# Kernel tuning notes

Measured on AMD Instinct MI355X. Metric: run time of the kernel, lower is better.

Reference implementation:

```python
import jax, jax.numpy as jnp
import numpy as np

B, L, S, H, E, D = 4, 2048, 2048, 8, 64, 64

def setup_inputs() -> dict:
    key = jax.random.key(0)
    kq, kk, kv = jax.random.split(key, 3)
    queries = jax.random.normal(kq, (B, L, H, E), dtype=jnp.float32)
    keys = jax.random.normal(kk, (B, S, H, E), dtype=jnp.float32)
    values = jax.random.normal(kv, (B, S, H, D), dtype=jnp.float32)
    return {"queries": queries, "keys": keys, "values": values}

def reference(queries, keys, values):
    # scale = self.scale or 1/sqrt(E)
    scale = 1.0 / jnp.sqrt(jnp.float32(queries.shape[-1]))
    # scores: [B, H, L, S]
    scores = jnp.einsum('blhe,bshe->bhls', queries, keys)
    # dropout is identity at inference (Keras Dropout only active in training)
    A = jax.nn.softmax(scale * scores, axis=-1)
    # output: [B, L, H, D]
    return jnp.einsum('bhls,bshd->blhd', A, values)
```

## Files before the change

kernel.cpp:

```cpp
#include <hip/hip_runtime.h>


#define B_ 4
#define L_ 2048
#define S_ 2048
#define H_ 8

#define NUMSZ (B_ * L_ * H_ * 64)
#define LSZ (B_ * L_ * H_)
#define KVELEM (B_ * H_ * S_ * 64)
#define TILE_ELEMS 2048

typedef __attribute__((ext_vector_type(8))) __bf16 bf16x8;
typedef __attribute__((ext_vector_type(4))) __bf16 bf16x4;
typedef __attribute__((ext_vector_type(16))) float floatx16;

union BF4U { bf16x4 v; uint2 u; };
union BF8U { bf16x8 v; uint4 u; };

__device__ __forceinline__ void async_load16(const void* g, void* l) {
  __builtin_amdgcn_global_load_lds(
      (const __attribute__((address_space(1))) unsigned int*)g,
      (__attribute__((address_space(3))) unsigned int*)l, 16, 0, 0);
}

__device__ __forceinline__ bf16x8 cvt8(float4 a, float4 b) {
  bf16x8 r;
  r[0] = (__bf16)a.x; r[1] = (__bf16)a.y; r[2] = (__bf16)a.z; r[3] = (__bf16)a.w;
  r[4] = (__bf16)b.x; r[5] = (__bf16)b.y; r[6] = (__bf16)b.z; r[7] = (__bf16)b.w;
  return r;
}

__device__ __forceinline__ void softmax_pb(const floatx16& sc, int h32, float& l,
                                           bf16x8& pB0v, bf16x8& pB1v) {
  BF4U pg[4];
#pragma unroll
  for (int g = 0; g < 4; ++g) {
    float p0 = __builtin_amdgcn_exp2f(sc[4 * g + 0]);
    float p1 = __builtin_amdgcn_exp2f(sc[4 * g + 1]);
    float p2 = __builtin_amdgcn_exp2f(sc[4 * g + 2]);
    float p3 = __builtin_amdgcn_exp2f(sc[4 * g + 3]);
    l += (p0 + p1) + (p2 + p3);
    pg[g].v = (bf16x4){(__bf16)p0, (__bf16)p1, (__bf16)p2, (__bf16)p3};
  }
  uint2 sendA = h32 ? pg[0].u : pg[1].u;
  uint2 sendB = h32 ? pg[2].u : pg[3].u;
  uint2 recvA, recvB;
  recvA.x = __shfl_xor((int)sendA.x, 32);
  recvA.y = __shfl_xor((int)sendA.y, 32);
  recvB.x = __shfl_xor((int)sendB.x, 32);
  recvB.y = __shfl_xor((int)sendB.y, 32);
  BF8U pB0, pB1;
  if (h32 == 0) {
    pB0.u = (uint4){pg[0].u.x, pg[0].u.y, recvA.x, recvA.y};
    pB1.u = (uint4){pg[2].u.x, pg[2].u.y, recvB.x, recvB.y};
  } else {
    pB0.u = (uint4){recvA.x, recvA.y, pg[1].u.x, pg[1].u.y};
    pB1.u = (uint4){recvB.x, recvB.y, pg[3].u.x, pg[3].u.y};
  }
  pB0v = pB0.v;
  pB1v = pB1.v;
}

__global__ __launch_bounds__(256) void prep_kernel(const float* __restrict__ K,
                                                   const float* __restrict__ V,
                                                   __bf16* __restrict__ Kb,
                                                   __bf16* __restrict__ Vb) {
  __shared__ float Vs[32 * 64];
  const int bid = blockIdx.x;
  const int xcd = bid & 7;
  const int idx = bid >> 3;
  const int pair = xcd * 4 + (idx >> 6);
  const int tile = idx & 63;
  const int h = pair & 7;
  const int b = pair >> 3;
  const int obid = pair * 64 + tile;
  const int s0 = tile * 32;
  const int i = threadIdx.x;

  {
    const int s = i >> 3, cp = i & 7;
    const int e0 = 8 * (cp ^ (s & 7));
    const float* src = K + (((size_t)(b * S_ + s0 + s) * H_ + h) * 64 + e0);
    float4 a = *(const float4*)src;
    float4 bb = *(const float4*)(src + 4);
    *(bf16x8*)(Kb + (size_t)obid * TILE_ELEMS + i * 8) = cvt8(a, bb);
  }
  {
    const int s = i >> 3, d0 = (i & 7) * 8;
    const float* src = V + (((size_t)(b * S_ + s0 + s) * H_ + h) * 64 + d0);
    float4 a = *(const float4*)src;
    float4 bb = *(const float4*)(src + 4);
    *(float4*)&Vs[s * 64 + d0] = a;
    *(float4*)&Vs[s * 64 + d0 + 4] = bb;
  }
  __syncthreads();
  {
    const int Ll = i >> 3, cp = i & 7;
    const int ci = cp ^ (Ll & 7);
    const int d = 2 * Ll + (ci >> 2);
    const int ch = ci & 3;
    BF8U o;
#pragma unroll
    for (int j = 0; j < 8; ++j) o.v[j] = (__bf16)Vs[(8 * ch + j) * 64 + d];
    *(bf16x8*)(Vb + (size_t)obid * TILE_ELEMS + i * 8) = o.v;
  }
}

__global__ __launch_bounds__(256, 3) void attn_kernel(const float* __restrict__ Q,
                                                      const __bf16* __restrict__ Kb,
                                                      const __bf16* __restrict__ Vb,
                                                      float* __restrict__ O,
                                                      float* __restrict__ num_ws,
                                                      float* __restrict__ l_ws,
                                                      int splits) {
  __shared__ __align__(16) __bf16 Kt[2][2 * TILE_ELEMS];
  __shared__ __align__(16) __bf16 Vt[2][2 * TILE_ELEMS];

  const int tid = threadIdx.x;
  const int lane = tid & 63;
  const int wave = tid >> 6;
  const int q32 = lane & 31;
  const int h32 = lane >> 5;

  const int bid = blockIdx.x;
  const int xcd = bid & 7;
  const int idx = bid >> 3;
  const int bs = 16 * splits;
  const int pairl = idx / bs;
  const int sub = idx - pairl * bs;
  const int pair = xcd * 4 + pairl;
  const int qb = sub & 15;
  const int split = sub >> 4;
  const int h = pair & 7;
  const int b = pair >> 3;

  const int NT2 = (S_ / 32) / splits / 2;
  const int tile0 = split * NT2 * 2;

  const float qscale = 0.125f * 1.44269504088896340736f;
  const int qrow = qb * 128 + wave * 32 + q32;
  bf16x8 qf[4];
  {
    const float* qp = Q + ((size_t)(b * L_ + qrow) * H_ + h) * 64;
#pragma unroll
    for (int c = 0; c < 4; ++c) {
      const float* p = qp + c * 16 + h32 * 8;
      float4 a = *(const float4*)p;
      float4 bb = *(const float4*)(p + 4);
      float t[8] = {a.x, a.y, a.z, a.w, bb.x, bb.y, bb.z, bb.w};
#pragma unroll
      for (int j = 0; j < 8; ++j) qf[c][j] = (__bf16)(t[j] * qscale);
    }
  }

  int koff[4];
#pragma unroll
  for (int c = 0; c < 4; ++c) koff[c] = (q32 * 8 + (((2 * c + h32) ^ (q32 & 7)))) * 8;
  int voff[2][2];
#pragma unroll
  for (int s2 = 0; s2 < 2; ++s2)
#pragma unroll
    for (int dt = 0; dt < 2; ++dt) {
      int dp = dt * 32 + q32;
      int Ll = dp >> 1;
      int ci = (dp & 1) * 4 + 2 * s2 + h32;
      voff[s2][dt] = (Ll * 8 + (ci ^ (Ll & 7))) * 8;
    }

  float l = 0.f;
  floatx16 ot[2];
#pragma unroll
  for (int r = 0; r < 16; ++r) { ot[0][r] = 0.f; ot[1][r] = 0.f; }

  const __bf16* KbBH = Kb + (size_t)(pair * 64) * TILE_ELEMS;
  const __bf16* VbBH = Vb + (size_t)(pair * 64) * TILE_ELEMS;
  const int lin8 = (wave * 64 + lane) * 8;

#pragma unroll
  for (int st = 0; st < 2; ++st) {
    async_load16(KbBH + (size_t)(tile0 + st) * TILE_ELEMS + lin8,
                 &Kt[0][st * TILE_ELEMS + wave * 512]);
    async_load16(VbBH + (size_t)(tile0 + st) * TILE_ELEMS + lin8,
                 &Vt[0][st * TILE_ELEMS + wave * 512]);
  }

  for (int t = 0; t < NT2; ++t) {
    const int buf = t & 1;
    __syncthreads();

    if (t + 1 < NT2) {
#pragma unroll
      for (int st = 0; st < 2; ++st) {
        async_load16(KbBH + (size_t)(tile0 + 2 * (t + 1) + st) * TILE_ELEMS + lin8,
                     &Kt[buf ^ 1][st * TILE_ELEMS + wave * 512]);
        async_load16(VbBH + (size_t)(tile0 + 2 * (t + 1) + st) * TILE_ELEMS + lin8,
                     &Vt[buf ^ 1][st * TILE_ELEMS + wave * 512]);
      }
    }

#pragma unroll
    for (int sb = 0; sb < 2; ++sb) {
      const __bf16* Kbuf = &Kt[buf][sb * TILE_ELEMS];
      const __bf16* Vbuf = &Vt[buf][sb * TILE_ELEMS];

      bf16x8 kA[4];
#pragma unroll
      for (int c = 0; c < 4; ++c) kA[c] = *(const bf16x8*)&Kbuf[koff[c]];

      floatx16 sc;
#pragma unroll
      for (int r = 0; r < 16; ++r) sc[r] = 0.f;
      __builtin_amdgcn_s_setprio(1);
#pragma unroll
      for (int c = 0; c < 4; ++c)
        sc = __builtin_amdgcn_mfma_f32_32x32x16_bf16(kA[c], qf[c], sc, 0, 0, 0);
      __builtin_amdgcn_s_setprio(0);

      bf16x8 p0, p1;
      softmax_pb(sc, h32, l, p0, p1);

      bf16x8 vA[4];
      vA[0] = *(const bf16x8*)&Vbuf[voff[0][0]];
      vA[1] = *(const bf16x8*)&Vbuf[voff[0][1]];
      vA[2] = *(const bf16x8*)&Vbuf[voff[1][0]];
      vA[3] = *(const bf16x8*)&Vbuf[voff[1][1]];
      __builtin_amdgcn_s_setprio(1);
      ot[0] = __builtin_amdgcn_mfma_f32_32x32x16_bf16(vA[0], p0, ot[0], 0, 0, 0);
      ot[1] = __builtin_amdgcn_mfma_f32_32x32x16_bf16(vA[1], p0, ot[1], 0, 0, 0);
      ot[0] = __builtin_amdgcn_mfma_f32_32x32x16_bf16(vA[2], p1, ot[0], 0, 0, 0);
      ot[1] = __builtin_amdgcn_mfma_f32_32x32x16_bf16(vA[3], p1, ot[1], 0, 0, 0);
      __builtin_amdgcn_s_setprio(0);
    }
  }

  {
    float lg = l + __shfl_xor(l, 32);
    if (splits == 1) {
      const float inv = 1.0f / lg;
      float* orow = O + ((size_t)(b * L_ + qrow) * H_ + h) * 64;
#pragma unroll
      for (int dt = 0; dt < 2; ++dt)
#pragma unroll
        for (int gg = 0; gg < 4; ++gg) {
          float4 v = {ot[dt][4 * gg + 0] * inv, ot[dt][4 * gg + 1] * inv,
                      ot[dt][4 * gg + 2] * inv, ot[dt][4 * gg + 3] * inv};
          *(float4*)(orow + dt * 32 + gg * 8 + h32 * 4) = v;
        }
    } else {
      float* nrow =
          num_ws + (size_t)split * NUMSZ + ((size_t)(b * L_ + qrow) * H_ + h) * 64;
#pragma unroll
      for (int dt = 0; dt < 2; ++dt)
#pragma unroll
        for (int gg = 0; gg < 4; ++gg) {
          float4 v = {ot[dt][4 * gg + 0], ot[dt][4 * gg + 1],
                      ot[dt][4 * gg + 2], ot[dt][4 * gg + 3]};
          *(float4*)(nrow + dt * 32 + gg * 8 + h32 * 4) = v;
        }
      if (h32 == 0)
        l_ws[(size_t)split * LSZ + (size_t)(b * L_ + qrow) * H_ + h] = lg;
    }
  }
}

__global__ __launch_bounds__(256) void combine_kernel(const float* __restrict__ num_ws,
                                                      const float* __restrict__ l_ws,
                                                      float* __restrict__ O, int splits) {
  const size_t i4 = ((size_t)blockIdx.x * 256 + threadIdx.x) * 4;
  float4 acc = {0.f, 0.f, 0.f, 0.f};
  float lt = 0.f;
  for (int s = 0; s < splits; ++s) {
    float4 v = *(const float4*)(num_ws + (size_t)s * NUMSZ + i4);
    acc.x += v.x; acc.y += v.y; acc.z += v.z; acc.w += v.w;
    lt += l_ws[(size_t)s * LSZ + (i4 >> 6)];
  }
  const float inv = 1.0f / lt;
  float4 o = {acc.x * inv, acc.y * inv, acc.z * inv, acc.w * inv};
  *(float4*)(O + i4) = o;
}

extern "C" void kernel_launch(void* const* d_in, const int* in_sizes, int n_in,
                              void* d_out, int out_size, void* d_ws, size_t ws_size,
                              hipStream_t stream) {
  const float* Q = (const float*)d_in[0];
  const float* K = (const float*)d_in[1];
  const float* V = (const float*)d_in[2];
  float* O = (float*)d_out;

  __bf16* Kb = (__bf16*)d_ws;
  __bf16* Vb = Kb + KVELEM;
  float* num_ws = (float*)(Vb + KVELEM);
  const size_t base = (size_t)2 * KVELEM * sizeof(__bf16);
  const size_t per_split = ((size_t)NUMSZ + (size_t)LSZ) * sizeof(float);
  int splits = 1;
  if (ws_size >= base + 4 * per_split) splits = 4;
  else if (ws_size >= base + 2 * per_split) splits = 2;
  float* l_ws = num_ws + (size_t)splits * NUMSZ;

  prep_kernel<<<B_ * H_ * 64, 256, 0, stream>>>(K, V, Kb, Vb);
  dim3 grid(B_ * H_ * (L_ / 128) * splits);
  attn_kernel<<<grid, 256, 0, stream>>>(Q, Kb, Vb, O, num_ws, l_ws, splits);
  if (splits > 1) {
    combine_kernel<<<NUMSZ / 4 / 256, 256, 0, stream>>>(num_ws, l_ws, O, splits);
  }
}
```

Baseline: 152.3 us.

## Fuse prep and attention into one cooperative kernel with grid sync

Merges the K/V bf16 conversion pass and the attention pass into a single cooperative kernel of 512 blocks that first does the prep tasks, then grid-syncs, then runs attention with splits=1. This removes separate kernel launches and the split-K combine pass. In exchange it gives up the split-S parallelism (512 blocks instead of up to 2048), adds a grid-wide barrier, and falls back to the old path if the cooperative launch fails.

```diff
diff --git a/kernel.cpp b/kernel.cpp
--- a/kernel.cpp
+++ b/kernel.cpp
@@ -1,4 +1,7 @@
 #include <hip/hip_runtime.h>
+#include <hip/hip_cooperative_groups.h>
+
+namespace cg = cooperative_groups;
 
 
 #define B_ 4
@@ -62,14 +65,12 @@
   pB1v = pB1.v;
 }
 
-__global__ __launch_bounds__(256) void prep_kernel(const float* __restrict__ K,
-                                                   const float* __restrict__ V,
-                                                   __bf16* __restrict__ Kb,
-                                                   __bf16* __restrict__ Vb) {
-  __shared__ float Vs[32 * 64];
-  const int bid = blockIdx.x;
-  const int xcd = bid & 7;
-  const int idx = bid >> 3;
+__device__ __forceinline__ void prep_task(int task, const float* __restrict__ K,
+                                          const float* __restrict__ V,
+                                          __bf16* __restrict__ Kb,
+                                          __bf16* __restrict__ Vb, float* Vs) {
+  const int xcd = task & 7;
+  const int idx = task >> 3;
   const int pair = xcd * 4 + (idx >> 6);
   const int tile = idx & 63;
   const int h = pair & 7;
@@ -105,27 +106,25 @@
     for (int j = 0; j < 8; ++j) o.v[j] = (__bf16)Vs[(8 * ch + j) * 64 + d];
     *(bf16x8*)(Vb + (size_t)obid * TILE_ELEMS + i * 8) = o.v;
   }
-}
-
-__global__ __launch_bounds__(256, 3) void attn_kernel(const float* __restrict__ Q,
-                                                      const __bf16* __restrict__ Kb,
-                                                      const __bf16* __restrict__ Vb,
-                                                      float* __restrict__ O,
-                                                      float* __restrict__ num_ws,
-                                                      float* __restrict__ l_ws,
-                                                      int splits) {
-  __shared__ __align__(16) __bf16 Kt[2][2 * TILE_ELEMS];
-  __shared__ __align__(16) __bf16 Vt[2][2 * TILE_ELEMS];
-
+  __syncthreads();
+}
+
+__device__ __forceinline__ void attn_task(int task, int splits,
+                                          const float* __restrict__ Q,
+                                          const __bf16* __restrict__ Kb,
+                                          const __bf16* __restrict__ Vb,
+                                          float* __restrict__ O,
+                                          float* __restrict__ num_ws,
+                                          float* __restrict__ l_ws,
+                                          __bf16* KtB, __bf16* VtB) {
   const int tid = threadIdx.x;
   const int lane = tid & 63;
   const int wave = tid >> 6;
   const int q32 = lane & 31;
   const int h32 = lane >> 5;
 
-  const int bid = blockIdx.x;
-  const int xcd = bid & 7;
-  const int idx = bid >> 3;
+  const int xcd = task & 7;
+  const int idx = task >> 3;
   const int bs = 16 * splits;
   const int pairl = idx / bs;
   const int sub = idx - pairl * bs;
@@ -180,9 +179,9 @@
 #pragma unroll
   for (int st = 0; st < 2; ++st) {
     async_load16(KbBH + (size_t)(tile0 + st) * TILE_ELEMS + lin8,
-                 &Kt[0][st * TILE_ELEMS + wave * 512]);
+                 KtB + st * TILE_ELEMS + wave * 512);
     async_load16(VbBH + (size_t)(tile0 + st) * TILE_ELEMS + lin8,
-                 &Vt[0][st * TILE_ELEMS + wave * 512]);
+                 VtB + st * TILE_ELEMS + wave * 512);
   }
 
   for (int t = 0; t < NT2; ++t) {
@@ -193,16 +192,16 @@
 #pragma unroll
       for (int st = 0; st < 2; ++st) {
         async_load16(KbBH + (size_t)(tile0 + 2 * (t + 1) + st) * TILE_ELEMS + lin8,
-                     &Kt[buf ^ 1][st * TILE_ELEMS + wave * 512]);
+                     KtB + (buf ^ 1) * (2 * TILE_ELEMS) + st * TILE_ELEMS + wave * 512);
         async_load16(VbBH + (size_t)(tile0 + 2 * (t + 1) + st) * TILE_ELEMS + lin8,
-                     &Vt[buf ^ 1][st * TILE_ELEMS + wave * 512]);
+                     VtB + (buf ^ 1) * (2 * TILE_ELEMS) + st * TILE_ELEMS + wave * 512);
       }
     }
 
 #pragma unroll
     for (int sb = 0; sb < 2; ++sb) {
-      const __bf16* Kbuf = &Kt[buf][sb * TILE_ELEMS];
-      const __bf16* Vbuf = &Vt[buf][sb * TILE_ELEMS];
+      const __bf16* Kbuf = KtB + buf * (2 * TILE_ELEMS) + sb * TILE_ELEMS;
+      const __bf16* Vbuf = VtB + buf * (2 * TILE_ELEMS) + sb * TILE_ELEMS;
 
       bf16x8 kA[4];
 #pragma unroll
@@ -264,6 +263,43 @@
   }
 }
 
+__global__ __launch_bounds__(256, 2) void fused_kernel(
+    const float* __restrict__ Q, const float* __restrict__ K,
+    const float* __restrict__ V, __bf16* __restrict__ Kb,
+    __bf16* __restrict__ Vb, float* __restrict__ O) {
+  __shared__ __align__(16) __bf16 Kt[2][2 * TILE_ELEMS];
+  __shared__ __align__(16) __bf16 Vt[2][2 * TILE_ELEMS];
+  const int bid = blockIdx.x;
+
+  for (int task = bid; task < B_ * H_ * 64; task += 512)
+    prep_task(task, K, V, Kb, Vb, (float*)&Kt[0][0]);
+
+  __threadfence();
+  cg::this_grid().sync();
+
+  attn_task(bid, 1, Q, Kb, Vb, O, nullptr, nullptr, &Kt[0][0], &Vt[0][0]);
+}
+
+__global__ __launch_bounds__(256) void prep_kernel(const float* __restrict__ K,
+                                                   const float* __restrict__ V,
+                                                   __bf16* __restrict__ Kb,
+                                                   __bf16* __restrict__ Vb) {
+  __shared__ float Vs[32 * 64];
+  prep_task(blockIdx.x, K, V, Kb, Vb, Vs);
+}
+
+__global__ __launch_bounds__(256, 3) void attn_kernel(const float* __restrict__ Q,
+                                                      const __bf16* __restrict__ Kb,
+                                                      const __bf16* __restrict__ Vb,
+                                                      float* __restrict__ O,
+                                                      float* __restrict__ num_ws,
+                                                      float* __restrict__ l_ws,
+                                                      int splits) {
+  __shared__ __align__(16) __bf16 Kt[2][2 * TILE_ELEMS];
+  __shared__ __align__(16) __bf16 Vt[2][2 * TILE_ELEMS];
+  attn_task(blockIdx.x, splits, Q, Kb, Vb, O, num_ws, l_ws, &Kt[0][0], &Vt[0][0]);
+}
+
 __global__ __launch_bounds__(256) void combine_kernel(const float* __restrict__ num_ws,
                                                       const float* __restrict__ l_ws,
                                                       float* __restrict__ O, int splits) {
@@ -290,6 +326,21 @@
 
   __bf16* Kb = (__bf16*)d_ws;
   __bf16* Vb = Kb + KVELEM;
+
+  {
+    void* args[6];
+    args[0] = (void*)&Q;
+    args[1] = (void*)&K;
+    args[2] = (void*)&V;
+    args[3] = (void*)&Kb;
+    args[4] = (void*)&Vb;
+    args[5] = (void*)&O;
+    hipError_t e = hipLaunchCooperativeKernel((const void*)fused_kernel, dim3(512),
+                                              dim3(256), (void**)args, 0, stream);
+    if (e == hipSuccess) return;
+    (void)hipGetLastError();
+  }
+
   float* num_ws = (float*)(Vb + KVELEM);
   const size_t base = (size_t)2 * KVELEM * sizeof(__bf16);
   const size_t per_split = ((size_t)NUMSZ + (size_t)LSZ) * sizeof(float);
```

Measured after the change: 236.0 us. +54.9%, slower.

## Use three uneven KV splits and interleave two QK tiles before softmax

Applied to the files above, without the earlier changes.

Changes the split-K count from four to three, with uneven tile ranges (11/11/10 double-tiles), so the grid is 1536 blocks instead of 2048. That reduces combine work and partial-result traffic and may suit the CU count better. The inner loop now issues both QK MFMA groups before either softmax, giving more independent MFMA work to overlap with the exp math. The cost is more live registers and some load imbalance across splits.

```diff
diff --git a/kernel.cpp b/kernel.cpp
--- a/kernel.cpp
+++ b/kernel.cpp
@@ -135,8 +135,14 @@
   const int h = pair & 7;
   const int b = pair >> 3;
 
-  const int NT2 = (S_ / 32) / splits / 2;
-  const int tile0 = split * NT2 * 2;
+  int nt2, tile0;
+  if (splits == 3) {
+    nt2 = (split < 2) ? 11 : 10;
+    tile0 = 22 * split;
+  } else {
+    nt2 = (S_ / 32) / (2 * splits);
+    tile0 = split * 2 * nt2;
+  }
 
   const float qscale = 0.125f * 1.44269504088896340736f;
   const int qrow = qb * 128 + wave * 32 + q32;
@@ -185,11 +191,11 @@
                  &Vt[0][st * TILE_ELEMS + wave * 512]);
   }
 
-  for (int t = 0; t < NT2; ++t) {
+  for (int t = 0; t < nt2; ++t) {
     const int buf = t & 1;
     __syncthreads();
 
-    if (t + 1 < NT2) {
+    if (t + 1 < nt2) {
 #pragma unroll
       for (int st = 0; st < 2; ++st) {
         async_load16(KbBH + (size_t)(tile0 + 2 * (t + 1) + st) * TILE_ELEMS + lin8,
@@ -199,37 +205,69 @@
       }
     }
 
-#pragma unroll
-    for (int sb = 0; sb < 2; ++sb) {
-      const __bf16* Kbuf = &Kt[buf][sb * TILE_ELEMS];
-      const __bf16* Vbuf = &Vt[buf][sb * TILE_ELEMS];
-
-      bf16x8 kA[4];
-#pragma unroll
-      for (int c = 0; c < 4; ++c) kA[c] = *(const bf16x8*)&Kbuf[koff[c]];
-
-      floatx16 sc;
-#pragma unroll
-      for (int r = 0; r < 16; ++r) sc[r] = 0.f;
+    const __bf16* Kbuf0 = &Kt[buf][0];
+    const __bf16* Kbuf1 = &Kt[buf][TILE_ELEMS];
+    const __bf16* Vbuf0 = &Vt[buf][0];
+    const __bf16* Vbuf1 = &Vt[buf][TILE_ELEMS];
+
+    floatx16 sc0;
+#pragma unroll
+    for (int r = 0; r < 16; ++r) sc0[r] = 0.f;
+    {
+      bf16x8 kA0[4];
+#pragma unroll
+      for (int c = 0; c < 4; ++c) kA0[c] = *(const bf16x8*)&Kbuf0[koff[c]];
       __builtin_amdgcn_s_setprio(1);
 #pragma unroll
       for (int c = 0; c < 4; ++c)
-        sc = __builtin_amdgcn_mfma_f32_32x32x16_bf16(kA[c], qf[c], sc, 0, 0, 0);
+        sc0 = __builtin_amdgcn_mfma_f32_32x32x16_bf16(kA0[c], qf[c], sc0, 0, 0, 0);
       __builtin_amdgcn_s_setprio(0);
-
-      bf16x8 p0, p1;
-      softmax_pb(sc, h32, l, p0, p1);
-
-      bf16x8 vA[4];
-      vA[0] = *(const bf16x8*)&Vbuf[voff[0][0]];
-      vA[1] = *(const bf16x8*)&Vbuf[voff[0][1]];
-      vA[2] = *(const bf16x8*)&Vbuf[voff[1][0]];
-      vA[3] = *(const bf16x8*)&Vbuf[voff[1][1]];
+    }
+    floatx16 sc1;
+#pragma unroll
+    for (int r = 0; r < 16; ++r) sc1[r] = 0.f;
+    {
+      bf16x8 kA1[4];
+#pragma unroll
+      for (int c = 0; c < 4; ++c) kA1[c] = *(const bf16x8*)&Kbuf1[koff[c]];
       __builtin_amdgcn_s_setprio(1);
-      ot[0] = __builtin_amdgcn_mfma_f32_32x32x16_bf16(vA[0], p0, ot[0], 0, 0, 0);
-      ot[1] = __builtin_amdgcn_mfma_f32_32x32x16_bf16(vA[1], p0, ot[1], 0, 0, 0);
-      ot[0] = __builtin_amdgcn_mfma_f32_32x32x16_bf16(vA[2], p1, ot[0], 0, 0, 0);
-      ot[1] = __builtin_amdgcn_mfma_f32_32x32x16_bf16(vA[3], p1, ot[1], 0, 0, 0);
+#pragma unroll
+      for (int c = 0; c < 4; ++c)
+        sc1 = __builtin_amdgcn_mfma_f32_32x32x16_bf16(kA1[c], qf[c], sc1, 0, 0, 0);
+      __builtin_amdgcn_s_setprio(0);
+    }
+
+    bf16x8 p00, p01;
+    softmax_pb(sc0, h32, l, p00, p01);
+
+    {
+      bf16x8 vA0[4];
+      vA0[0] = *(const bf16x8*)&Vbuf0[voff[0][0]];
+      vA0[1] = *(const bf16x8*)&Vbuf0[voff[0][1]];
+      vA0[2] = *(const bf16x8*)&Vbuf0[voff[1][0]];
+      vA0[3] = *(const bf16x8*)&Vbuf0[voff[1][1]];
+      __builtin_amdgcn_s_setprio(1);
+      ot[0] = __builtin_amdgcn_mfma_f32_32x32x16_bf16(vA0[0], p00, ot[0], 0, 0, 0);
+      ot[1] = __builtin_amdgcn_mfma_f32_32x32x16_bf16(vA0[1], p00, ot[1], 0, 0, 0);
+      ot[0] = __builtin_amdgcn_mfma_f32_32x32x16_bf16(vA0[2], p01, ot[0], 0, 0, 0);
+      ot[1] = __builtin_amdgcn_mfma_f32_32x32x16_bf16(vA0[3], p01, ot[1], 0, 0, 0);
+      __builtin_amdgcn_s_setprio(0);
+    }
+
+    bf16x8 p10, p11;
+    softmax_pb(sc1, h32, l, p10, p11);
+
+    {
+      bf16x8 vA1[4];
+      vA1[0] = *(const bf16x8*)&Vbuf1[voff[0][0]];
+      vA1[1] = *(const bf16x8*)&Vbuf1[voff[0][1]];
+      vA1[2] = *(const bf16x8*)&Vbuf1[voff[1][0]];
+      vA1[3] = *(const bf16x8*)&Vbuf1[voff[1][1]];
+      __builtin_amdgcn_s_setprio(1);
+      ot[0] = __builtin_amdgcn_mfma_f32_32x32x16_bf16(vA1[0], p10, ot[0], 0, 0, 0);
+      ot[1] = __builtin_amdgcn_mfma_f32_32x32x16_bf16(vA1[1], p10, ot[1], 0, 0, 0);
+      ot[0] = __builtin_amdgcn_mfma_f32_32x32x16_bf16(vA1[2], p11, ot[0], 0, 0, 0);
+      ot[1] = __builtin_amdgcn_mfma_f32_32x32x16_bf16(vA1[3], p11, ot[1], 0, 0, 0);
       __builtin_amdgcn_s_setprio(0);
     }
   }
@@ -294,12 +332,12 @@
   const size_t base = (size_t)2 * KVELEM * sizeof(__bf16);
   const size_t per_split = ((size_t)NUMSZ + (size_t)LSZ) * sizeof(float);
   int splits = 1;
-  if (ws_size >= base + 4 * per_split) splits = 4;
+  if (ws_size >= base + 3 * per_split) splits = 3;
   else if (ws_size >= base + 2 * per_split) splits = 2;
   float* l_ws = num_ws + (size_t)splits * NUMSZ;
 
   prep_kernel<<<B_ * H_ * 64, 256, 0, stream>>>(K, V, Kb, Vb);
-  dim3 grid(B_ * H_ * (L_ / 128) * splits);
+  dim3 grid(B_ * H_ * 16 * splits);
   attn_kernel<<<grid, 256, 0, stream>>>(Q, Kb, Vb, O, num_ws, l_ws, splits);
   if (splits > 1) {
     combine_kernel<<<NUMSZ / 4 / 256, 256, 0, stream>>>(num_ws, l_ws, O, splits);
```

Result: faster. 148.0 us (-2.8%).
